# Kernel optimization log

Measured on AMD Instinct MI355X. Metric: run time of the kernel, lower is better.

## Reference

```python
import jax, jax.numpy as jnp
import numpy as np

B = 4096   # batch
NE = 512   # n_embed (codebook size)


def _quantize(x, embed):
    """VQ-VAE style quantizer. x: [..., dim], embed: [dim, n_embed].
    Returns (straight-through quantized x, commitment diff, code ids)."""
    dim = embed.shape[0]
    flat = x.reshape(-1, dim)
    # squared euclidean distance to every codeword (single stable expansion)
    dist = ((flat * flat).sum(1, keepdims=True)
            - 2.0 * (flat @ embed)
            + (embed * embed).sum(0, keepdims=True))
    idx = jnp.argmin(dist, axis=1)
    q = jnp.take(embed.T, idx, axis=0).reshape(x.shape)
    diff = jnp.mean((jax.lax.stop_gradient(q) - x) ** 2)
    q_st = x + jax.lax.stop_gradient(q - x)  # straight-through estimator
    return q_st, diff, idx


def setup_inputs() -> dict:
    key = jax.random.key(0)
    ks = jax.random.split(key, 7)
    return {
        "x": jax.random.normal(ks[0], (B, 784), jnp.float32),
        "W1": jax.random.normal(ks[1], (512, 784), jnp.float32) * 0.03,   # fc1.weight [out,in]
        "W2": jax.random.normal(ks[2], (512, 512), jnp.float32) * 0.04,   # fc2.weight [out,in]
        "W3": jax.random.normal(ks[3], (10, 512), jnp.float32) * 0.04,    # fc3.weight [out,in]
        "gamma1": jnp.ones((512,), jnp.float32),   # bn1.weight
        "beta1": jnp.zeros((512,), jnp.float32),   # bn1.bias
        "embed_fq21": jax.random.normal(ks[4], (8, NE), jnp.float32),          # fq21 codebook [dim, n_embed]
        "embed_q2": jax.random.normal(ks[5], (16, NE), jnp.float32) * 0.04,    # quant2 codebook
        "embed_fq22": jax.random.normal(ks[6], (2, NE), jnp.float32),          # fq22 codebook
    }


def reference(x, W1, W2, W3, gamma1, beta1, embed_fq21, embed_q2, embed_fq22):
    Bsz = x.shape[0]
    # fc1 (no bias) + relu
    h = jax.nn.relu(x @ W1.T)                                   # [B, 512]
    # fq21: x.view(B, 8, 64).permute(0, 2, 1) -> [B, 64, 8] strided groups
    xg = h.reshape(Bsz, 8, 64).transpose(0, 2, 1)
    q1, d_f21, _ = _quantize(xg, embed_fq21)
    qx = q1.transpose(0, 2, 1).reshape(Bsz, 512)                # [B, 512]

    # weight_quantization(fc2, quant2, in_mem=8, out_mem=2), fully vectorized:
    # groups[g, c, i, o] = W2.T[c*8+i, g*2+o]
    Wt = W2.T                                                   # [in=512, out=512]
    groups = Wt.reshape(64, 8, 256, 2).transpose(2, 0, 1, 3)    # [256, 64, 8, 2]
    qw, d2, _ = _quantize(groups.reshape(256, 64, 16), embed_q2)
    # scatter back: qW2[g*2+o, c*8+i] = qw[g, c, 2i+o]  (torch back_weights layout)
    qW2 = qw.reshape(256, 64, 8, 2).transpose(0, 3, 1, 2).reshape(512, 512)
    qW2 = jax.lax.stop_gradient(qW2)  # torch assigns via .data (detached copy)

    # bn1 in training mode (batch statistics, biased variance, eps=1e-5)
    mu = qx.mean(0)
    var = jnp.mean((qx - mu) ** 2, axis=0)
    xn = (qx - mu) * jax.lax.rsqrt(var + 1e-5) * gamma1 + beta1
    h2 = jax.nn.relu(xn @ qW2.T)                                # [B, 512]

    # fq22: x.view(B, 2, 256).permute(0, 2, 1) -> [B, 256, 2]
    xg2 = h2.reshape(Bsz, 2, 256).transpose(0, 2, 1)
    q2f, d_f22, _ = _quantize(xg2, embed_fq22)
    qx2 = q2f.transpose(0, 2, 1).reshape(Bsz, 512)

    out = qx2 @ W3.T                                            # [B, 10]
    return out, d_f21 + d_f22 + d2
```

## Files before the change

kernel.cpp:

```cpp
#include <hip/hip_runtime.h>
#include <math.h>

constexpr int BATCH = 4096;
constexpr int D_IN  = 784;
constexpr int F     = 512;
constexpr int NEC   = 512;

constexpr int   GRID_N = 64;
constexpr float GCELL  = 0.25f;
constexpr int   GCAP   = 96;

__global__ __launch_bounds__(256) void k_gridprep(
    const float* __restrict__ E3, float* __restrict__ ecb3,
    int* __restrict__ gcnt, short* __restrict__ glist)
{
    __shared__ float ex[NEC], ey[NEC];
    const int t = threadIdx.x;
    for (int i = t; i < NEC; i += 256) {
        ex[i] = E3[i];
        ey[i] = E3[NEC + i];
    }
    __syncthreads();
    const int gid = blockIdx.x * 256 + t;
    if (gid < NEC) {
        float a0 = ex[gid], a1 = ey[gid];
        float cn = __fadd_rn(__fmul_rn(a0, a0), __fmul_rn(a1, a1));
        reinterpret_cast<float4*>(ecb3)[gid] = make_float4(a0, a1, cn, 0.f);
    }
    const int wv = t >> 6, l = t & 63;
    const int cell = blockIdx.x * 4 + wv;
    const int cx = cell & (GRID_N - 1), cy = cell >> 6;
    const float x0 = cx * GCELL, x1 = x0 + GCELL;
    const float y0 = cy * GCELL, y1 = y0 + GCELL;
    float mU = 3.4e38f;
    #pragma unroll
    for (int j = 0; j < 8; ++j) {
        const int n = j * 64 + l;
        float exn = ex[n], eyn = ey[n];
        float dxmax = fmaxf(x1 - exn, exn - x0);
        float dymax = fmaxf(y1 - eyn, eyn - y0);
        mU = fminf(mU, dxmax * dxmax + dymax * dymax);
    }
    #pragma unroll
    for (int off = 32; off; off >>= 1) mU = fminf(mU, __shfl_xor(mU, off));
    const float thr = mU + 0.01f;
    int cnt = 0;
    short* lst = glist + (size_t)cell * GCAP;
    #pragma unroll
    for (int j = 0; j < 8; ++j) {
        const int n = j * 64 + l;
        float exn = ex[n], eyn = ey[n];
        float dxmin = fmaxf(fmaxf(x0 - exn, exn - x1), 0.f);
        float dymin = fmaxf(fmaxf(y0 - eyn, eyn - y1), 0.f);
        const bool acc = (dxmin * dxmin + dymin * dymin <= thr);
        unsigned long long mask = __ballot(acc);
        if (acc) {
            int pos = cnt + __popcll(mask & ((1ull << l) - 1ull));
            if (pos < GCAP) lst[pos] = (short)n;
        }
        cnt += __popcll(mask);
    }
    if (l == 0) gcnt[cell] = cnt;
}

template<bool RELU, bool BN>
__global__ __launch_bounds__(256, 2) void k_gemm_np(
    const float* __restrict__ A, const float* __restrict__ Bw, float* __restrict__ C,
    int M, int N, int K, int KC,
    const float* __restrict__ mu, const float* __restrict__ rs,
    const float* __restrict__ gamma, const float* __restrict__ beta)
{
    __shared__ float As[2][16][68];
    __shared__ float Bs[2][16][68];
    const int t  = threadIdx.x;
    const int nwgy = gridDim.y;
    const int bid  = blockIdx.y * 8 + blockIdx.x;
    const int swz  = (bid & 7) * nwgy + (bid >> 3);
    const int bm = (swz >> 3) * 64, bn = (swz & 7) * 64;
    const int tm = (t >> 4) * 4, tn = (t & 15) * 4;
    const int rA = t >> 2;
    const int c4 = (t & 3) * 4;
    const float* Arow = A + (size_t)(bm + rA) * K + c4;
    const float* Brow = Bw + (size_t)(bn + rA) * K + c4;

    float tot[4][4];
    float accp[4][4] = {};
    bool first = true;

    {
        float4 af = *reinterpret_cast<const float4*>(Arow);
        float4 bf = *reinterpret_cast<const float4*>(Brow);
        float av[4] = {af.x, af.y, af.z, af.w};
        if (BN) {
            #pragma unroll
            for (int u = 0; u < 4; ++u) {
                const int k = c4 + u;
                float d = __fsub_rn(av[u], mu[k]);
                d = __fmul_rn(d, rs[k]);
                d = __fmul_rn(d, gamma[k]);
                av[u] = __fadd_rn(d, beta[k]);
            }
        }
        As[0][c4 + 0][rA] = av[0]; As[0][c4 + 1][rA] = av[1];
        As[0][c4 + 2][rA] = av[2]; As[0][c4 + 3][rA] = av[3];
        Bs[0][c4 + 0][rA] = bf.x;  Bs[0][c4 + 1][rA] = bf.y;
        Bs[0][c4 + 2][rA] = bf.z;  Bs[0][c4 + 3][rA] = bf.w;
    }
    __syncthreads();

    int cur = 0;
    for (int k0 = 0; k0 < K; k0 += 16) {
        const bool has_next = (k0 + 16) < K;
        float4 a_p, b_p;
        if (has_next) {
            a_p = *reinterpret_cast<const float4*>(Arow + k0 + 16);
            b_p = *reinterpret_cast<const float4*>(Brow + k0 + 16);
        }
        #pragma unroll
        for (int kk = 0; kk < 16; ++kk) {
            float4 a4 = *reinterpret_cast<const float4*>(&As[cur][kk][tm]);
            float4 b4 = *reinterpret_cast<const float4*>(&Bs[cur][kk][tn]);
            float aa[4] = {a4.x, a4.y, a4.z, a4.w};
            float bb[4] = {b4.x, b4.y, b4.z, b4.w};
            #pragma unroll
            for (int i = 0; i < 4; ++i)
                #pragma unroll
                for (int j = 0; j < 4; ++j)
                    accp[i][j] = fmaf(aa[i], bb[j], accp[i][j]);
        }
        if (has_next) {
            float av[4] = {a_p.x, a_p.y, a_p.z, a_p.w};
            if (BN) {
                #pragma unroll
                for (int u = 0; u < 4; ++u) {
                    const int k = k0 + 16 + c4 + u;
                    float d = __fsub_rn(av[u], mu[k]);
                    d = __fmul_rn(d, rs[k]);
                    d = __fmul_rn(d, gamma[k]);
                    av[u] = __fadd_rn(d, beta[k]);
                }
            }
            const int alt = cur ^ 1;
            As[alt][c4 + 0][rA] = av[0]; As[alt][c4 + 1][rA] = av[1];
            As[alt][c4 + 2][rA] = av[2]; As[alt][c4 + 3][rA] = av[3];
            Bs[alt][c4 + 0][rA] = b_p.x; Bs[alt][c4 + 1][rA] = b_p.y;
            Bs[alt][c4 + 2][rA] = b_p.z; Bs[alt][c4 + 3][rA] = b_p.w;
        }
        __syncthreads();
        const int kend = k0 + 16;
        if ((kend % KC) == 0 || kend == K) {
            #pragma unroll
            for (int i = 0; i < 4; ++i)
                #pragma unroll
                for (int j = 0; j < 4; ++j) {
                    tot[i][j] = first ? accp[i][j] : __fadd_rn(tot[i][j], accp[i][j]);
                    accp[i][j] = 0.f;
                }
            first = false;
        }
        cur ^= 1;
    }
    #pragma unroll
    for (int i = 0; i < 4; ++i) {
        float r0 = RELU ? fmaxf(tot[i][0], 0.f) : tot[i][0];
        float r1 = RELU ? fmaxf(tot[i][1], 0.f) : tot[i][1];
        float r2 = RELU ? fmaxf(tot[i][2], 0.f) : tot[i][2];
        float r3 = RELU ? fmaxf(tot[i][3], 0.f) : tot[i][3];
        float4 r = make_float4(r0, r1, r2, r3);
        *reinterpret_cast<float4*>(&C[(size_t)(bm + tm + i) * N + bn + tn]) = r;
    }
}

__device__ __forceinline__ double wave_reduce_add(double v) {
    #pragma unroll
    for (int off = 32; off; off >>= 1) v += __shfl_xor(v, off);
    return v;
}

__device__ __forceinline__ void block_partial(double dsum, double* pbuf) {
    __shared__ double wsum[4];
    const int t = threadIdx.x;
    dsum = wave_reduce_add(dsum);
    if ((t & 63) == 0) wsum[t >> 6] = dsum;
    __syncthreads();
    if (t == 0)
        pbuf[blockIdx.x] = ((wsum[0] + wsum[1]) + wsum[2]) + wsum[3];
}

__global__ __launch_bounds__(256) void k_fq21_np(
    const float* __restrict__ h, const float* __restrict__ E,
    float* __restrict__ qx, double* __restrict__ pbuf)
{
    __shared__ float Es[NEC][8];
    __shared__ float Cn[NEC];
    const int t = threadIdx.x;
    for (int i = t; i < 8 * NEC; i += 256) Es[i & (NEC - 1)][i >> 9] = E[i];
    __syncthreads();
    for (int n = t; n < NEC; n += 256) {
        float c = __fmul_rn(Es[n][0], Es[n][0]);
        #pragma unroll
        for (int j = 1; j < 8; ++j)
            c = __fadd_rn(c, __fmul_rn(Es[n][j], Es[n][j]));
        Cn[n] = c;
    }
    __syncthreads();
    const int idx = blockIdx.x * 256 + t;
    const int b = idx >> 6, c = idx & 63;
    const float* hb = h + (size_t)b * F + c;
    float v[8];
    #pragma unroll
    for (int j = 0; j < 8; ++j) v[j] = hb[j * 64];
    float s[8];
    #pragma unroll
    for (int j = 0; j < 8; ++j) s[j] = __fmul_rn(v[j], v[j]);
    const float Aterm = __fadd_rn(
        __fadd_rn(__fadd_rn(s[0], s[1]), __fadd_rn(s[2], s[3])),
        __fadd_rn(__fadd_rn(s[4], s[5]), __fadd_rn(s[6], s[7])));
    float best = 3.4e38f; int bi = 0;
    for (int n = 0; n < NEC; ++n) {
        float4 e0 = *reinterpret_cast<const float4*>(&Es[n][0]);
        float4 e1 = *reinterpret_cast<const float4*>(&Es[n][4]);
        float bsum = __fmul_rn(v[0], e0.x);
        bsum = fmaf(v[1], e0.y, bsum);
        bsum = fmaf(v[2], e0.z, bsum);
        bsum = fmaf(v[3], e0.w, bsum);
        bsum = fmaf(v[4], e1.x, bsum);
        bsum = fmaf(v[5], e1.y, bsum);
        bsum = fmaf(v[6], e1.z, bsum);
        bsum = fmaf(v[7], e1.w, bsum);
        float d = __fadd_rn(__fsub_rn(Aterm, __fadd_rn(bsum, bsum)), Cn[n]);
        if (d < best) { best = d; bi = n; }
    }
    float4 q0 = *reinterpret_cast<const float4*>(&Es[bi][0]);
    float4 q1 = *reinterpret_cast<const float4*>(&Es[bi][4]);
    float bq[8] = {q0.x, q0.y, q0.z, q0.w, q1.x, q1.y, q1.z, q1.w};
    double dsum = 0.0;
    float* qb = qx + (size_t)b * F + c;
    #pragma unroll
    for (int j = 0; j < 8; ++j) {
        float df = __fsub_rn(bq[j], v[j]);
        dsum += (double)df * (double)df;
        qb[j * 64] = __fadd_rn(v[j], df);
    }
    block_partial(dsum, pbuf);
}

__global__ __launch_bounds__(256) void k_wq_np(
    const float* __restrict__ W2, const float* __restrict__ E,
    float* __restrict__ qW2, double* __restrict__ pbuf)
{
    __shared__ float Es[NEC][16];
    __shared__ float Cn[NEC];
    const int t = threadIdx.x;
    for (int i = t; i < 16 * NEC; i += 256) Es[i & (NEC - 1)][i >> 9] = E[i];
    __syncthreads();
    for (int n = t; n < NEC; n += 256) {
        float c = __fmul_rn(Es[n][0], Es[n][0]);
        #pragma unroll
        for (int j = 1; j < 16; ++j)
            c = __fadd_rn(c, __fmul_rn(Es[n][j], Es[n][j]));
        Cn[n] = c;
    }
    __syncthreads();
    const int idx = blockIdx.x * 256 + t;
    const int g = idx >> 6, c = idx & 63;
    float v[16];
    #pragma unroll
    for (int k = 0; k < 16; ++k)
        v[k] = W2[(size_t)(2 * g + (k & 1)) * F + 8 * c + (k >> 1)];
    float s[16];
    #pragma unroll
    for (int k = 0; k < 16; ++k) s[k] = __fmul_rn(v[k], v[k]);
    float r[8];
    #pragma unroll
    for (int j = 0; j < 8; ++j) r[j] = __fadd_rn(s[j], s[j + 8]);
    const float Aterm = __fadd_rn(
        __fadd_rn(__fadd_rn(r[0], r[1]), __fadd_rn(r[2], r[3])),
        __fadd_rn(__fadd_rn(r[4], r[5]), __fadd_rn(r[6], r[7])));
    float best = 3.4e38f; int bi = 0;
    for (int n = 0; n < NEC; ++n) {
        float bsum = __fmul_rn(v[0], Es[n][0]);
        #pragma unroll
        for (int k = 1; k < 16; ++k) bsum = fmaf(v[k], Es[n][k], bsum);
        float d = __fadd_rn(__fsub_rn(Aterm, __fadd_rn(bsum, bsum)), Cn[n]);
        if (d < best) { best = d; bi = n; }
    }
    double dsum = 0.0;
    #pragma unroll
    for (int k = 0; k < 16; ++k) {
        float df = __fsub_rn(Es[bi][k], v[k]);
        dsum += (double)df * (double)df;
        qW2[(size_t)(2 * g + (k & 1)) * F + 8 * c + (k >> 1)] = __fadd_rn(v[k], df);
    }
    block_partial(dsum, pbuf);
}

__global__ __launch_bounds__(256) void k_transpose(
    const float* __restrict__ qx, float* __restrict__ qxT)
{
    __shared__ float tile[64][65];
    const int t = threadIdx.x;
    const int bx = blockIdx.x * 64;
    const int by = blockIdx.y * 64;
    const int r = t >> 4, c4 = (t & 15) * 4;
    #pragma unroll
    for (int s = 0; s < 4; ++s) {
        float4 v = *reinterpret_cast<const float4*>(&qx[(size_t)(by + r + s * 16) * F + bx + c4]);
        tile[r + s * 16][c4 + 0] = v.x; tile[r + s * 16][c4 + 1] = v.y;
        tile[r + s * 16][c4 + 2] = v.z; tile[r + s * 16][c4 + 3] = v.w;
    }
    __syncthreads();
    const int fo = t >> 4, b4 = (t & 15) * 4;
    #pragma unroll
    for (int s = 0; s < 4; ++s) {
        float4 v;
        v.x = tile[b4 + 0][fo + s * 16];
        v.y = tile[b4 + 1][fo + s * 16];
        v.z = tile[b4 + 2][fo + s * 16];
        v.w = tile[b4 + 3][fo + s * 16];
        *reinterpret_cast<float4*>(&qxT[(size_t)(bx + fo + s * 16) * BATCH + by + b4]) = v;
    }
}

__global__ __launch_bounds__(64) void k_bn(
    const float* __restrict__ qxT, float* __restrict__ mu, float* __restrict__ rs)
{
    const int t = threadIdx.x;
    if (t >= 16) return;
    const int f = blockIdx.x * 16 + t;
    const float4* rp = reinterpret_cast<const float4*>(qxT + (size_t)f * BATCH);

    float4 b0[4], b1[4], b2[4], b3[4], b4[4], b5[4], b6[4], b7[4];

#define BN_LD(B, c)                                                          \
    { _Pragma("unroll") for (int q = 0; q < 4; ++q) B[q] = rp[(c) * 4 + q]; }
#define BN_SUM(B)                                                            \
    { _Pragma("unroll") for (int q = 0; q < 4; ++q) {                        \
        acc = __fadd_rn(acc, B[q].x); acc = __fadd_rn(acc, B[q].y);          \
        acc = __fadd_rn(acc, B[q].z); acc = __fadd_rn(acc, B[q].w); } }
#define BN_VAR(B)                                                            \
    { _Pragma("unroll") for (int q = 0; q < 4; ++q) { float d_;              \
        d_ = __fsub_rn(B[q].x, m); acc2 = __fadd_rn(acc2, __fmul_rn(d_, d_));\
        d_ = __fsub_rn(B[q].y, m); acc2 = __fadd_rn(acc2, __fmul_rn(d_, d_));\
        d_ = __fsub_rn(B[q].z, m); acc2 = __fadd_rn(acc2, __fmul_rn(d_, d_));\
        d_ = __fsub_rn(B[q].w, m); acc2 = __fadd_rn(acc2, __fmul_rn(d_, d_)); } }

    float acc = 0.f;
    BN_LD(b0, 0) BN_LD(b1, 1) BN_LD(b2, 2) BN_LD(b3, 3)
    BN_LD(b4, 4) BN_LD(b5, 5) BN_LD(b6, 6)
    for (int g = 0; g < 31; ++g) {
        BN_LD(b7, 8 * g + 7)  BN_SUM(b0)
        BN_LD(b0, 8 * g + 8)  BN_SUM(b1)
        BN_LD(b1, 8 * g + 9)  BN_SUM(b2)
        BN_LD(b2, 8 * g + 10) BN_SUM(b3)
        BN_LD(b3, 8 * g + 11) BN_SUM(b4)
        BN_LD(b4, 8 * g + 12) BN_SUM(b5)
        BN_LD(b5, 8 * g + 13) BN_SUM(b6)
        BN_LD(b6, 8 * g + 14) BN_SUM(b7)
    }
    BN_LD(b7, 255)
    BN_SUM(b0) BN_SUM(b1) BN_SUM(b2) BN_SUM(b3)
    BN_SUM(b4) BN_SUM(b5) BN_SUM(b6) BN_SUM(b7)
    const float m = __fmul_rn(acc, 1.f / 4096.f);

    float acc2 = 0.f;
    BN_LD(b0, 0) BN_LD(b1, 1) BN_LD(b2, 2) BN_LD(b3, 3)
    BN_LD(b4, 4) BN_LD(b5, 5) BN_LD(b6, 6)
    for (int g = 0; g < 31; ++g) {
        BN_LD(b7, 8 * g + 7)  BN_VAR(b0)
        BN_LD(b0, 8 * g + 8)  BN_VAR(b1)
        BN_LD(b1, 8 * g + 9)  BN_VAR(b2)
        BN_LD(b2, 8 * g + 10) BN_VAR(b3)
        BN_LD(b3, 8 * g + 11) BN_VAR(b4)
        BN_LD(b4, 8 * g + 12) BN_VAR(b5)
        BN_LD(b5, 8 * g + 13) BN_VAR(b6)
        BN_LD(b6, 8 * g + 14) BN_VAR(b7)
    }
    BN_LD(b7, 255)
    BN_VAR(b0) BN_VAR(b1) BN_VAR(b2) BN_VAR(b3)
    BN_VAR(b4) BN_VAR(b5) BN_VAR(b6) BN_VAR(b7)
#undef BN_LD
#undef BN_SUM
#undef BN_VAR
    float var = __fmul_rn(acc2, 1.f / 4096.f);
    float w = __fadd_rn(var, 1e-5f);
    mu[f] = m;
    rs[f] = __fdiv_rn(1.0f, __fsqrt_rn(w));
}

__global__ __launch_bounds__(256) void k_fq22_np(
    const float* __restrict__ h2, const float* __restrict__ ecb3,
    const int* __restrict__ gcnt, const short* __restrict__ glist,
    float* __restrict__ qx2, double* __restrict__ pbuf)
{
    __shared__ float4 EsL[NEC];
    const int t = threadIdx.x;
    for (int n = t; n < NEC; n += 256)
        EsL[n] = reinterpret_cast<const float4*>(ecb3)[n];
    __syncthreads();
    const int b = blockIdx.x;
    const float v0 = h2[(size_t)b * F + t];
    const float v1 = h2[(size_t)b * F + 256 + t];
    const float Aterm = __fadd_rn(__fmul_rn(v0, v0), __fmul_rn(v1, v1));
    float best = 3.4e38f; int bi = 0;
    const bool inbox = (v0 < 16.f) && (v1 < 16.f);
    int cx = (int)(v0 * 4.f), cy = (int)(v1 * 4.f);
    int cell = (cy << 6) + cx;
    int cnt = inbox ? gcnt[cell] : (NEC + 1);
    if (cnt <= GCAP) {
        const short* lst = glist + (size_t)cell * GCAP;
        int i = 0;
        const int cnt4 = cnt & ~3;
        for (; i < cnt4; i += 4) {
            ushort4 ids = *reinterpret_cast<const ushort4*>(lst + i);
            float4 ea = EsL[ids.x];
            float4 eb = EsL[ids.y];
            float4 ec = EsL[ids.z];
            float4 ed = EsL[ids.w];
            float ba = fmaf(v1, ea.y, __fmul_rn(v0, ea.x));
            float da = __fadd_rn(__fsub_rn(Aterm, __fadd_rn(ba, ba)), ea.z);
            if (da < best) { best = da; bi = ids.x; }
            float bb = fmaf(v1, eb.y, __fmul_rn(v0, eb.x));
            float db = __fadd_rn(__fsub_rn(Aterm, __fadd_rn(bb, bb)), eb.z);
            if (db < best) { best = db; bi = ids.y; }
            float bc = fmaf(v1, ec.y, __fmul_rn(v0, ec.x));
            float dc = __fadd_rn(__fsub_rn(Aterm, __fadd_rn(bc, bc)), ec.z);
            if (dc < best) { best = dc; bi = ids.z; }
            float bd = fmaf(v1, ed.y, __fmul_rn(v0, ed.x));
            float dd = __fadd_rn(__fsub_rn(Aterm, __fadd_rn(bd, bd)), ed.z);
            if (dd < best) { best = dd; bi = ids.w; }
        }
        for (; i < cnt; ++i) {
            int id = lst[i];
            float4 e = EsL[id];
            float bsum = fmaf(v1, e.y, __fmul_rn(v0, e.x));
            float d = __fadd_rn(__fsub_rn(Aterm, __fadd_rn(bsum, bsum)), e.z);
            if (d < best) { best = d; bi = id; }
        }
    } else {
        for (int n = 0; n < NEC; ++n) {
            float4 e = EsL[n];
            float bsum = fmaf(v1, e.y, __fmul_rn(v0, e.x));
            float d = __fadd_rn(__fsub_rn(Aterm, __fadd_rn(bsum, bsum)), e.z);
            if (d < best) { best = d; bi = n; }
        }
    }
    float4 eb = EsL[bi];
    float d0 = __fsub_rn(eb.x, v0), d1 = __fsub_rn(eb.y, v1);
    qx2[(size_t)b * F + t]       = __fadd_rn(v0, d0);
    qx2[(size_t)b * F + 256 + t] = __fadd_rn(v1, d1);
    block_partial((double)d0 * d0 + (double)d1 * d1, pbuf);
}

__global__ __launch_bounds__(256) void k_gemm3(
    const float* __restrict__ qx2, const float* __restrict__ W3, float* __restrict__ out,
    const double* __restrict__ p21, const double* __restrict__ pwq,
    const double* __restrict__ p22)
{
    const int t = threadIdx.x;
    if (blockIdx.x == gridDim.x - 1) {
        __shared__ double sd[256];
        __shared__ double res[2];
        double s = 0.0;
        for (int i = t; i < 1024; i += 256) s += p21[i];
        sd[t] = s; __syncthreads();
        for (int o = 128; o; o >>= 1) { if (t < o) sd[t] += sd[t + o]; __syncthreads(); }
        if (t == 0) res[0] = sd[0];
        __syncthreads();
        s = (t < 64) ? pwq[t] : 0.0;
        sd[t] = s; __syncthreads();
        for (int o = 128; o; o >>= 1) { if (t < o) sd[t] += sd[t + o]; __syncthreads(); }
        if (t == 0) res[1] = sd[0];
        __syncthreads();
        s = 0.0;
        for (int i = t; i < 4096; i += 256) s += p22[i];
        sd[t] = s; __syncthreads();
        for (int o = 128; o; o >>= 1) { if (t < o) sd[t] += sd[t + o]; __syncthreads(); }
        if (t == 0) {
            double d21 = res[0] * (1.0 / 2097152.0);
            double dq  = res[1] * (1.0 / 262144.0);
            double d22 = sd[0]  * (1.0 / 2097152.0);
            out[BATCH * 10] = (float)((d21 + d22) + dq);
        }
        return;
    }
    __shared__ float Ws[10 * F];
    for (int i = t; i < 10 * F; i += 256) Ws[i] = W3[i];
    __syncthreads();
    const int w = t >> 6, l = t & 63;
    const int b = blockIdx.x * 4 + w;
    const float* xb = qx2 + (size_t)b * F;
    double acc[10] = {};
    for (int i = l; i < F; i += 64) {
        double xv = (double)xb[i];
        #pragma unroll
        for (int o = 0; o < 10; ++o) acc[o] = fma(xv, (double)Ws[o * F + i], acc[o]);
    }
    #pragma unroll
    for (int o = 0; o < 10; ++o) {
        double a = wave_reduce_add(acc[o]);
        if (l == 0) out[(size_t)b * 10 + o] = (float)a;
    }
}

extern "C" void kernel_launch(void* const* d_in, const int* in_sizes, int n_in,
                              void* d_out, int out_size, void* d_ws, size_t ws_size,
                              hipStream_t stream)
{
    const float* x     = (const float*)d_in[0];
    const float* W1    = (const float*)d_in[1];
    const float* W2    = (const float*)d_in[2];
    const float* W3    = (const float*)d_in[3];
    const float* gamma = (const float*)d_in[4];
    const float* beta  = (const float*)d_in[5];
    const float* E1    = (const float*)d_in[6];
    const float* E2    = (const float*)d_in[7];
    const float* E3    = (const float*)d_in[8];
    float* out = (float*)d_out;

    const int KC = 512;

    char* ws = (char*)d_ws;
    float*  hf    = (float*)ws;
    float*  qxf   = (float*)(ws + (size_t) 8 * 1024 * 1024);
    float*  qW2f  = (float*)(ws + (size_t)16 * 1024 * 1024);
    float*  muf   = (float*)(ws + (size_t)17 * 1024 * 1024);
    float*  rsf   = muf + F;
    float*  ecb3  = (float*)(ws + (size_t)17 * 1024 * 1024 + 8192);
    int*    gcnt  = (int*)(ws + (size_t)18 * 1024 * 1024);
    short*  glist = (short*)(ws + (size_t)18 * 1024 * 1024 + 16384);
    double* p21   = (double*)(ws + (size_t)19 * 1024 * 1024);
    double* pwq   = p21 + 1024;
    double* p22   = pwq + 64;
    float*  qxT   = (float*)(ws + (size_t)20 * 1024 * 1024);

    k_gridprep<<<1024, 256, 0, stream>>>(E3, ecb3, gcnt, glist);
    k_gemm_np<true, false><<<dim3(F / 64, BATCH / 64), 256, 0, stream>>>(
        x, W1, hf, BATCH, F, D_IN, KC, nullptr, nullptr, nullptr, nullptr);
    k_fq21_np<<<BATCH * 64 / 256, 256, 0, stream>>>(hf, E1, qxf, p21);
    k_wq_np<<<64, 256, 0, stream>>>(W2, E2, qW2f, pwq);
    k_transpose<<<dim3(F / 64, BATCH / 64), 256, 0, stream>>>(qxf, qxT);
    k_bn<<<32, 64, 0, stream>>>(qxT, muf, rsf);
    k_gemm_np<true, true><<<dim3(F / 64, BATCH / 64), 256, 0, stream>>>(
        qxf, qW2f, hf, BATCH, F, F, KC, muf, rsf, gamma, beta);
    k_fq22_np<<<BATCH, 256, 0, stream>>>(hf, ecb3, gcnt, glist, qxf, p22);
    k_gemm3<<<BATCH / 4 + 1, 256, 0, stream>>>(qxf, W3, out, p21, pwq, p22);
}
```

Baseline: 288.5 us.

## Merge weight-quantize into grid-prep kernel and use 8x4 GEMM microtiles with 128 threads

Folds the codebook weight quantization kernel into the grid-prep launch as 64 extra blocks, removing one kernel launch and letting the work overlap with grid construction. The FP32 GEMM now runs 128 threads per block, with each thread computing an 8x4 output microtile instead of 4x4. This raises register-level reuse and halves the threads per tile. The risk is lower occupancy and latency hiding, and the merged blocks are unbalanced.

```diff
diff --git a/kernel.cpp b/kernel.cpp
--- a/kernel.cpp
+++ b/kernel.cpp
@@ -10,12 +10,77 @@
 constexpr float GCELL  = 0.25f;
 constexpr int   GCAP   = 96;
 
-__global__ __launch_bounds__(256) void k_gridprep(
+__device__ __forceinline__ double wave_reduce_add(double v) {
+    #pragma unroll
+    for (int off = 32; off; off >>= 1) v += __shfl_xor(v, off);
+    return v;
+}
+
+__device__ __forceinline__ void block_partial_idx(double dsum, double* pbuf, int idx) {
+    __shared__ double wsum[4];
+    const int t = threadIdx.x;
+    dsum = wave_reduce_add(dsum);
+    if ((t & 63) == 0) wsum[t >> 6] = dsum;
+    __syncthreads();
+    if (t == 0)
+        pbuf[idx] = ((wsum[0] + wsum[1]) + wsum[2]) + wsum[3];
+}
+
+__global__ __launch_bounds__(256) void k_prep_wq(
     const float* __restrict__ E3, float* __restrict__ ecb3,
-    int* __restrict__ gcnt, short* __restrict__ glist)
-{
+    int* __restrict__ gcnt, short* __restrict__ glist,
+    const float* __restrict__ W2, const float* __restrict__ E2,
+    float* __restrict__ qW2, double* __restrict__ pwq)
+{
+    const int t = threadIdx.x;
+    if (blockIdx.x >= 1024) {
+        const int wb = blockIdx.x - 1024;
+        __shared__ float Es[NEC][16];
+        __shared__ float Cn[NEC];
+        for (int i = t; i < 16 * NEC; i += 256) Es[i & (NEC - 1)][i >> 9] = E2[i];
+        __syncthreads();
+        for (int n = t; n < NEC; n += 256) {
+            float c = __fmul_rn(Es[n][0], Es[n][0]);
+            #pragma unroll
+            for (int j = 1; j < 16; ++j)
+                c = __fadd_rn(c, __fmul_rn(Es[n][j], Es[n][j]));
+            Cn[n] = c;
+        }
+        __syncthreads();
+        const int idx = wb * 256 + t;
+        const int g = idx >> 6, c = idx & 63;
+        float v[16];
+        #pragma unroll
+        for (int k = 0; k < 16; ++k)
+            v[k] = W2[(size_t)(2 * g + (k & 1)) * F + 8 * c + (k >> 1)];
+        float s[16];
+        #pragma unroll
+        for (int k = 0; k < 16; ++k) s[k] = __fmul_rn(v[k], v[k]);
+        float r[8];
+        #pragma unroll
+        for (int j = 0; j < 8; ++j) r[j] = __fadd_rn(s[j], s[j + 8]);
+        const float Aterm = __fadd_rn(
+            __fadd_rn(__fadd_rn(r[0], r[1]), __fadd_rn(r[2], r[3])),
+            __fadd_rn(__fadd_rn(r[4], r[5]), __fadd_rn(r[6], r[7])));
+        float best = 3.4e38f; int bi = 0;
+        for (int n = 0; n < NEC; ++n) {
+            float bsum = __fmul_rn(v[0], Es[n][0]);
+            #pragma unroll
+            for (int k = 1; k < 16; ++k) bsum = fmaf(v[k], Es[n][k], bsum);
+            float d = __fadd_rn(__fsub_rn(Aterm, __fadd_rn(bsum, bsum)), Cn[n]);
+            if (d < best) { best = d; bi = n; }
+        }
+        double dsum = 0.0;
+        #pragma unroll
+        for (int k = 0; k < 16; ++k) {
+            float df = __fsub_rn(Es[bi][k], v[k]);
+            dsum += (double)df * (double)df;
+            qW2[(size_t)(2 * g + (k & 1)) * F + 8 * c + (k >> 1)] = __fadd_rn(v[k], df);
+        }
+        block_partial_idx(dsum, pwq, wb);
+        return;
+    }
     __shared__ float ex[NEC], ey[NEC];
-    const int t = threadIdx.x;
     for (int i = t; i < NEC; i += 256) {
         ex[i] = E3[i];
         ey[i] = E3[NEC + i];
@@ -64,7 +129,7 @@
 }
 
 template<bool RELU, bool BN>
-__global__ __launch_bounds__(256, 2) void k_gemm_np(
+__global__ __launch_bounds__(128, 2) void k_gemm_np(
     const float* __restrict__ A, const float* __restrict__ Bw, float* __restrict__ C,
     int M, int N, int K, int KC,
     const float* __restrict__ mu, const float* __restrict__ rs,
@@ -77,80 +142,79 @@
     const int bid  = blockIdx.y * 8 + blockIdx.x;
     const int swz  = (bid & 7) * nwgy + (bid >> 3);
     const int bm = (swz >> 3) * 64, bn = (swz & 7) * 64;
-    const int tm = (t >> 4) * 4, tn = (t & 15) * 4;
-    const int rA = t >> 2;
-    const int c4 = (t & 3) * 4;
-    const float* Arow = A + (size_t)(bm + rA) * K + c4;
-    const float* Brow = Bw + (size_t)(bn + rA) * K + c4;
-
-    float tot[4][4];
-    float accp[4][4] = {};
+    const int tm = (t >> 4) * 8, tn = (t & 15) * 4;
+    const int rA = t >> 1;
+    const int c8 = (t & 1) * 8;
+    const float* Arow = A + (size_t)(bm + rA) * K + c8;
+    const float* Brow = Bw + (size_t)(bn + rA) * K + c8;
+
+    float tot[8][4];
+    float accp[8][4] = {};
     bool first = true;
 
+#define GEMM_BNX(val, kidx)                                   \
+    if (BN) {                                                 \
+        float d_ = __fsub_rn(val, mu[kidx]);                  \
+        d_ = __fmul_rn(d_, rs[kidx]);                         \
+        d_ = __fmul_rn(d_, gamma[kidx]);                      \
+        val = __fadd_rn(d_, beta[kidx]);                      \
+    }
+
     {
-        float4 af = *reinterpret_cast<const float4*>(Arow);
-        float4 bf = *reinterpret_cast<const float4*>(Brow);
-        float av[4] = {af.x, af.y, af.z, af.w};
-        if (BN) {
-            #pragma unroll
-            for (int u = 0; u < 4; ++u) {
-                const int k = c4 + u;
-                float d = __fsub_rn(av[u], mu[k]);
-                d = __fmul_rn(d, rs[k]);
-                d = __fmul_rn(d, gamma[k]);
-                av[u] = __fadd_rn(d, beta[k]);
-            }
-        }
-        As[0][c4 + 0][rA] = av[0]; As[0][c4 + 1][rA] = av[1];
-        As[0][c4 + 2][rA] = av[2]; As[0][c4 + 3][rA] = av[3];
-        Bs[0][c4 + 0][rA] = bf.x;  Bs[0][c4 + 1][rA] = bf.y;
-        Bs[0][c4 + 2][rA] = bf.z;  Bs[0][c4 + 3][rA] = bf.w;
+        float4 a0 = *reinterpret_cast<const float4*>(Arow);
+        float4 a1 = *reinterpret_cast<const float4*>(Arow + 4);
+        float4 b0 = *reinterpret_cast<const float4*>(Brow);
+        float4 b1 = *reinterpret_cast<const float4*>(Brow + 4);
+        float av[8] = {a0.x, a0.y, a0.z, a0.w, a1.x, a1.y, a1.z, a1.w};
+        float bv[8] = {b0.x, b0.y, b0.z, b0.w, b1.x, b1.y, b1.z, b1.w};
+        #pragma unroll
+        for (int e = 0; e < 8; ++e) {
+            GEMM_BNX(av[e], c8 + e)
+            As[0][c8 + e][rA] = av[e];
+            Bs[0][c8 + e][rA] = bv[e];
+        }
     }
     __syncthreads();
 
     int cur = 0;
     for (int k0 = 0; k0 < K; k0 += 16) {
         const bool has_next = (k0 + 16) < K;
-        float4 a_p, b_p;
+        float4 a0p, a1p, b0p, b1p;
         if (has_next) {
-            a_p = *reinterpret_cast<const float4*>(Arow + k0 + 16);
-            b_p = *reinterpret_cast<const float4*>(Brow + k0 + 16);
+            a0p = *reinterpret_cast<const float4*>(Arow + k0 + 16);
+            a1p = *reinterpret_cast<const float4*>(Arow + k0 + 20);
+            b0p = *reinterpret_cast<const float4*>(Brow + k0 + 16);
+            b1p = *reinterpret_cast<const float4*>(Brow + k0 + 20);
         }
         #pragma unroll
         for (int kk = 0; kk < 16; ++kk) {
-            float4 a4 = *reinterpret_cast<const float4*>(&As[cur][kk][tm]);
-            float4 b4 = *reinterpret_cast<const float4*>(&Bs[cur][kk][tn]);
-            float aa[4] = {a4.x, a4.y, a4.z, a4.w};
+            float4 alo = *reinterpret_cast<const float4*>(&As[cur][kk][tm]);
+            float4 ahi = *reinterpret_cast<const float4*>(&As[cur][kk][tm + 4]);
+            float4 b4  = *reinterpret_cast<const float4*>(&Bs[cur][kk][tn]);
+            float aa[8] = {alo.x, alo.y, alo.z, alo.w, ahi.x, ahi.y, ahi.z, ahi.w};
             float bb[4] = {b4.x, b4.y, b4.z, b4.w};
             #pragma unroll
-            for (int i = 0; i < 4; ++i)
+            for (int i = 0; i < 8; ++i)
                 #pragma unroll
                 for (int j = 0; j < 4; ++j)
                     accp[i][j] = fmaf(aa[i], bb[j], accp[i][j]);
         }
         if (has_next) {
-            float av[4] = {a_p.x, a_p.y, a_p.z, a_p.w};
-            if (BN) {
-                #pragma unroll
-                for (int u = 0; u < 4; ++u) {
-                    const int k = k0 + 16 + c4 + u;
-                    float d = __fsub_rn(av[u], mu[k]);
-                    d = __fmul_rn(d, rs[k]);
-                    d = __fmul_rn(d, gamma[k]);
-                    av[u] = __fadd_rn(d, beta[k]);
-                }
+            float av[8] = {a0p.x, a0p.y, a0p.z, a0p.w, a1p.x, a1p.y, a1p.z, a1p.w};
+            float bv[8] = {b0p.x, b0p.y, b0p.z, b0p.w, b1p.x, b1p.y, b1p.z, b1p.w};
+            const int alt = cur ^ 1;
+            #pragma unroll
+            for (int e = 0; e < 8; ++e) {
+                GEMM_BNX(av[e], k0 + 16 + c8 + e)
+                As[alt][c8 + e][rA] = av[e];
+                Bs[alt][c8 + e][rA] = bv[e];
             }
-            const int alt = cur ^ 1;
-            As[alt][c4 + 0][rA] = av[0]; As[alt][c4 + 1][rA] = av[1];
-            As[alt][c4 + 2][rA] = av[2]; As[alt][c4 + 3][rA] = av[3];
-            Bs[alt][c4 + 0][rA] = b_p.x; Bs[alt][c4 + 1][rA] = b_p.y;
-            Bs[alt][c4 + 2][rA] = b_p.z; Bs[alt][c4 + 3][rA] = b_p.w;
         }
         __syncthreads();
         const int kend = k0 + 16;
         if ((kend % KC) == 0 || kend == K) {
             #pragma unroll
-            for (int i = 0; i < 4; ++i)
+            for (int i = 0; i < 8; ++i)
                 #pragma unroll
                 for (int j = 0; j < 4; ++j) {
                     tot[i][j] = first ? accp[i][j] : __fadd_rn(tot[i][j], accp[i][j]);
@@ -160,31 +224,16 @@
         }
         cur ^= 1;
     }
-    #pragma unroll
-    for (int i = 0; i < 4; ++i) {
-        float r0 = RELU ? fmaxf(tot[i][0], 0.f) : tot[i][0];
-        float r1 = RELU ? fmaxf(tot[i][1], 0.f) : tot[i][1];
-        float r2 = RELU ? fmaxf(tot[i][2], 0.f) : tot[i][2];
-        float r3 = RELU ? fmaxf(tot[i][3], 0.f) : tot[i][3];
-        float4 r = make_float4(r0, r1, r2, r3);
+#undef GEMM_BNX
+    #pragma unroll
+    for (int i = 0; i < 8; ++i) {
+        float4 r;
+        r.x = RELU ? fmaxf(tot[i][0], 0.f) : tot[i][0];
+        r.y = RELU ? fmaxf(tot[i][1], 0.f) : tot[i][1];
+        r.z = RELU ? fmaxf(tot[i][2], 0.f) : tot[i][2];
+        r.w = RELU ? fmaxf(tot[i][3], 0.f) : tot[i][3];
         *reinterpret_cast<float4*>(&C[(size_t)(bm + tm + i) * N + bn + tn]) = r;
     }
-}
-
-__device__ __forceinline__ double wave_reduce_add(double v) {
-    #pragma unroll
-    for (int off = 32; off; off >>= 1) v += __shfl_xor(v, off);
-    return v;
-}
-
-__device__ __forceinline__ void block_partial(double dsum, double* pbuf) {
-    __shared__ double wsum[4];
-    const int t = threadIdx.x;
-    dsum = wave_reduce_add(dsum);
-    if ((t & 63) == 0) wsum[t >> 6] = dsum;
-    __syncthreads();
-    if (t == 0)
-        pbuf[blockIdx.x] = ((wsum[0] + wsum[1]) + wsum[2]) + wsum[3];
 }
 
 __global__ __launch_bounds__(256) void k_fq21_np(
@@ -242,57 +291,7 @@
         dsum += (double)df * (double)df;
         qb[j * 64] = __fadd_rn(v[j], df);
     }
-    block_partial(dsum, pbuf);
-}
-
-__global__ __launch_bounds__(256) void k_wq_np(
-    const float* __restrict__ W2, const float* __restrict__ E,
-    float* __restrict__ qW2, double* __restrict__ pbuf)
-{
-    __shared__ float Es[NEC][16];
-    __shared__ float Cn[NEC];
-    const int t = threadIdx.x;
-    for (int i = t; i < 16 * NEC; i += 256) Es[i & (NEC - 1)][i >> 9] = E[i];
-    __syncthreads();
-    for (int n = t; n < NEC; n += 256) {
-        float c = __fmul_rn(Es[n][0], Es[n][0]);
-        #pragma unroll
-        for (int j = 1; j < 16; ++j)
-            c = __fadd_rn(c, __fmul_rn(Es[n][j], Es[n][j]));
-        Cn[n] = c;
-    }
-    __syncthreads();
-    const int idx = blockIdx.x * 256 + t;
-    const int g = idx >> 6, c = idx & 63;
-    float v[16];
-    #pragma unroll
-    for (int k = 0; k < 16; ++k)
-        v[k] = W2[(size_t)(2 * g + (k & 1)) * F + 8 * c + (k >> 1)];
-    float s[16];
-    #pragma unroll
-    for (int k = 0; k < 16; ++k) s[k] = __fmul_rn(v[k], v[k]);
-    float r[8];
-    #pragma unroll
-    for (int j = 0; j < 8; ++j) r[j] = __fadd_rn(s[j], s[j + 8]);
-    const float Aterm = __fadd_rn(
-        __fadd_rn(__fadd_rn(r[0], r[1]), __fadd_rn(r[2], r[3])),
-        __fadd_rn(__fadd_rn(r[4], r[5]), __fadd_rn(r[6], r[7])));
-    float best = 3.4e38f; int bi = 0;
-    for (int n = 0; n < NEC; ++n) {
-        float bsum = __fmul_rn(v[0], Es[n][0]);
-        #pragma unroll
-        for (int k = 1; k < 16; ++k) bsum = fmaf(v[k], Es[n][k], bsum);
-        float d = __fadd_rn(__fsub_rn(Aterm, __fadd_rn(bsum, bsum)), Cn[n]);
-        if (d < best) { best = d; bi = n; }
-    }
-    double dsum = 0.0;
-    #pragma unroll
-    for (int k = 0; k < 16; ++k) {
-        float df = __fsub_rn(Es[bi][k], v[k]);
-        dsum += (double)df * (double)df;
-        qW2[(size_t)(2 * g + (k & 1)) * F + 8 * c + (k >> 1)] = __fadd_rn(v[k], df);
-    }
-    block_partial(dsum, pbuf);
+    block_partial_idx(dsum, pbuf, blockIdx.x);
 }
 
 __global__ __launch_bounds__(256) void k_transpose(
@@ -449,7 +448,7 @@
     float d0 = __fsub_rn(eb.x, v0), d1 = __fsub_rn(eb.y, v1);
     qx2[(size_t)b * F + t]       = __fadd_rn(v0, d0);
     qx2[(size_t)b * F + 256 + t] = __fadd_rn(v1, d1);
-    block_partial((double)d0 * d0 + (double)d1 * d1, pbuf);
+    block_partial_idx((double)d0 * d0 + (double)d1 * d1, pbuf, blockIdx.x);
 }
 
 __global__ __launch_bounds__(256) void k_gemm3(
@@ -534,14 +533,13 @@
     double* p22   = pwq + 64;
     float*  qxT   = (float*)(ws + (size_t)20 * 1024 * 1024);
 
-    k_gridprep<<<1024, 256, 0, stream>>>(E3, ecb3, gcnt, glist);
-    k_gemm_np<true, false><<<dim3(F / 64, BATCH / 64), 256, 0, stream>>>(
+    k_prep_wq<<<1088, 256, 0, stream>>>(E3, ecb3, gcnt, glist, W2, E2, qW2f, pwq);
+    k_gemm_np<true, false><<<dim3(F / 64, BATCH / 64), 128, 0, stream>>>(
         x, W1, hf, BATCH, F, D_IN, KC, nullptr, nullptr, nullptr, nullptr);
     k_fq21_np<<<BATCH * 64 / 256, 256, 0, stream>>>(hf, E1, qxf, p21);
-    k_wq_np<<<64, 256, 0, stream>>>(W2, E2, qW2f, pwq);
     k_transpose<<<dim3(F / 64, BATCH / 64), 256, 0, stream>>>(qxf, qxT);
     k_bn<<<32, 64, 0, stream>>>(qxT, muf, rsf);
-    k_gemm_np<true, true><<<dim3(F / 64, BATCH / 64), 256, 0, stream>>>(
+    k_gemm_np<true, true><<<dim3(F / 64, BATCH / 64), 128, 0, stream>>>(
         qxf, qW2f, hf, BATCH, F, F, KC, muf, rsf, gamma, beta);
     k_fq22_np<<<BATCH, 256, 0, stream>>>(hf, ecb3, gcnt, glist, qxf, p22);
     k_gemm3<<<BATCH / 4 + 1, 256, 0, stream>>>(qxf, W3, out, p21, pwq, p22);
```

Result: slower. 417.7 us (+44.8%).
